# Performance work log

Hardware: AMD Instinct MI355X
Metric: run time of the kernel (lower is better)

## Reference

```python
import jax, jax.numpy as jnp
import numpy as np
from jax import lax

EMB, HID, L, PATCH, IMG, K = 192, 64, 6, 4, 224, 8
FMAP = IMG // PATCH
N = FMAP * FMAP
B = 8
ALG = 4
GB_np = np.array([0, 1, 1, 2])  # grade of each blade [1, e1, e2, e12]
GB = jnp.asarray(GB_np)

def _cayley_np():
    C = np.zeros((4, 4, 4), np.float32)
    tbl = {(0,0):(0,1.),(0,1):(1,1.),(0,2):(2,1.),(0,3):(3,1.),
           (1,0):(1,1.),(1,1):(0,1.),(1,2):(3,1.),(1,3):(2,1.),
           (2,0):(2,1.),(2,1):(3,-1.),(2,2):(0,1.),(2,3):(1,-1.),
           (3,0):(3,1.),(3,1):(2,-1.),(3,2):(1,1.),(3,3):(0,-1.)}
    for (i, j), (k, s) in tbl.items():
        C[i, j, k] = s
    return C

CAY_np = _cayley_np()
CAYLEY = jnp.asarray(CAY_np)
_paths = np.zeros((3, 3, 3), bool)
for _i in range(4):
    for _j in range(4):
        for _k in range(4):
            if CAY_np[_i, _j, _k] != 0:
                _paths[GB_np[_i], GB_np[_j], GB_np[_k]] = True
PI, PJ, PK = (jnp.asarray(a) for a in np.nonzero(_paths))
NPATH = int(_paths.sum())  # 10 geometric-product paths for Cl(2,0)

def build_knn_graph(H, W, k):
    yy, xx = np.meshgrid(np.arange(H, dtype=np.float32), np.arange(W, dtype=np.float32), indexing='ij')
    coords = np.stack([xx.ravel(), yy.ravel()], -1)
    cn = coords / np.array([W - 1, H - 1], np.float32) * 2 - 1
    d = np.linalg.norm(cn[:, None] - cn[None], axis=-1)
    np.fill_diagonal(d, np.inf)
    idx = np.argsort(d, axis=-1, kind='stable')[:, :k]
    rows = np.repeat(np.arange(H * W), k)
    cols = idx.reshape(-1)
    return rows.astype(np.int32), cols.astype(np.int32), cn.astype(np.float32)

def mvlin(x, W, b=None):
    # per-grade MVLinear: W [out,in,3] expanded to blades via GB
    y = jnp.einsum('nmi,bmi->bni', W[:, :, GB], x)
    if b is not None:
        y = y.at[:, :, 0].add(b)  # bias embedded in scalar blade only
    return y

def mvlin_flat(x, W, b):
    # subspaces=False MVLinear: same weight across blades
    y = jnp.einsum('nm,bmi->bni', W, x)
    return y.at[:, :, 0].add(b)

def mv_silu(x, a, b):
    # invariants: [scalar, q(grade1), q(grade2)]; gate = sigmoid(a*inv+b)
    inv = jnp.concatenate([x[..., :1], x[..., 1:2]**2 + x[..., 2:3]**2, x[..., 3:4]**2], -1)
    return jax.nn.sigmoid(a * inv + b)[..., GB] * x

def normalize_mv(x, a):
    q = jnp.concatenate([x[..., :1]**2, x[..., 1:2]**2 + x[..., 2:3]**2, x[..., 3:4]**2], -1)
    n = jnp.sqrt(q + 1e-12)
    d = jax.nn.sigmoid(a) * (n - 1.0) + 1.0
    return x / (d + 1e-6)[..., GB]

def sgp(x, Wl, bl, Wr, na, gw):
    # SteerableGeometricProductLayer
    xr = normalize_mv(mvlin(x, Wr), na)
    full = jnp.zeros((gw.shape[0], 3, 3, 3), x.dtype).at[:, PI, PJ, PK].set(gw)
    fb = full[:, GB][:, :, GB][:, :, :, GB]  # [feat,4,4,4]
    gp = jnp.einsum('bni,nijk,bnk->bnj', x, CAYLEY[None] * fb, xr)
    return (mvlin(x, Wl, bl) + gp) * np.float32(1.0 / np.sqrt(2.0))

def _forward(x, conv_w, conv_b, stem_g, stem_b, pos_embed, in_W, in_b, in_Wl, in_bl, in_Wr, in_na, in_gw, eg_eW, eg_eb, eg_sa, eg_sb, eg_nW, eg_nb, eg_Wl, eg_bl, eg_Wr, eg_na, eg_gw, eg_aa, eg_ab, out_W, out_b, on_g, on_b, cls_W, cls_b, coords, rows, cols):
    Bx = x.shape[0]
    # stem: strided conv + LayerNorm over (C,H,W)
    y = lax.conv_general_dilated(x, conv_w, (PATCH, PATCH), 'VALID', dimension_numbers=('NCHW', 'OIHW', 'NCHW')) + conv_b[None, :, None, None]
    mu = y.mean(axis=(1, 2, 3), keepdims=True)
    var = ((y - mu) ** 2).mean(axis=(1, 2, 3), keepdims=True)
    y = (y - mu) / jnp.sqrt(var + 1e-5) * stem_g[None] + stem_b[None]
    y = y + pos_embed
    feat = y.transpose(0, 2, 3, 1).reshape(Bx * N, EMB)
    # embed features in scalar blade, coordinates in vector blades e1,e2
    h = jnp.zeros((Bx * N, EMB + 1, ALG), x.dtype)
    h = h.at[:, :EMB, 0].set(feat)
    h = h.at[:, EMB, 1:3].set(jnp.tile(coords, (Bx, 1)))
    h = sgp(mvlin_flat(h, in_W, in_b), in_Wl, in_bl, in_Wr, in_na, in_gw)
    BN = Bx * N
    for i in range(L):
        m = mv_silu(mvlin(h[rows] - h[cols], eg_eW[i], eg_eb[i]), eg_sa[i], eg_sb[i])
        agg = jax.ops.segment_sum(m, rows, num_segments=BN)  # count computed but unused in original
        nu = mvlin(jnp.concatenate([h, agg], axis=1), eg_nW[i], eg_nb[i])
        out = mv_silu(sgp(nu, eg_Wl[i], eg_bl[i], eg_Wr[i], eg_na[i], eg_gw[i]), eg_aa[i], eg_ab[i])
        h = h + out if i > 0 else out
    s = mvlin_flat(h, out_W, out_b)[..., 0]
    mu2 = s.mean(-1, keepdims=True)
    v2 = ((s - mu2) ** 2).mean(-1, keepdims=True)
    s = (s - mu2) / jnp.sqrt(v2 + 1e-5) * on_g + on_b
    pooled = s.reshape(Bx, N, EMB).mean(axis=1)
    return pooled @ cls_W.T + cls_b

def setup_inputs() -> dict:
    key = jax.random.key(0)
    ks = iter(jax.random.split(key, 64))
    nrm = lambda shape, s=0.05: jax.random.normal(next(ks), shape, jnp.float32) * s
    rows, cols, cn = build_knn_graph(FMAP, FMAP, K)
    offs = np.arange(B, dtype=np.int32)[:, None] * N
    rows_b = (rows[None] + offs).reshape(-1)
    cols_b = (cols[None] + offs).reshape(-1)
    return dict(
        x=jax.random.normal(next(ks), (B, 3, IMG, IMG), jnp.float32),
        conv_w=nrm((EMB, 3, PATCH, PATCH)),
        conv_b=jnp.zeros((EMB,), jnp.float32),
        stem_g=jnp.ones((EMB, FMAP, FMAP), jnp.float32),
        stem_b=jnp.zeros((EMB, FMAP, FMAP), jnp.float32),
        pos_embed=nrm((1, EMB, FMAP, FMAP), 0.02),
        coords=jnp.asarray(cn),
        in_W=nrm((HID, EMB + 1)), in_b=jnp.zeros((HID,), jnp.float32),
        in_Wl=nrm((HID, HID, 3)), in_bl=jnp.zeros((HID,), jnp.float32),
        in_Wr=nrm((HID, HID, 3)), in_na=jnp.zeros((HID, 3), jnp.float32),
        in_gw=nrm((HID, NPATH), 0.2),
        eg_eW=nrm((L, HID, HID, 3)), eg_eb=jnp.zeros((L, HID), jnp.float32),
        eg_sa=jnp.ones((L, HID, 3), jnp.float32), eg_sb=jnp.zeros((L, HID, 3), jnp.float32),
        eg_nW=nrm((L, HID, 2 * HID, 3)), eg_nb=jnp.zeros((L, HID), jnp.float32),
        eg_Wl=nrm((L, HID, HID, 3)), eg_bl=jnp.zeros((L, HID), jnp.float32),
        eg_Wr=nrm((L, HID, HID, 3)), eg_na=jnp.zeros((L, HID, 3), jnp.float32),
        eg_gw=nrm((L, HID, NPATH), 0.2),
        eg_aa=jnp.ones((L, HID, 3), jnp.float32), eg_ab=jnp.zeros((L, HID, 3), jnp.float32),
        out_W=nrm((EMB, HID)), out_b=jnp.zeros((EMB,), jnp.float32),
        on_g=jnp.ones((EMB,), jnp.float32), on_b=jnp.zeros((EMB,), jnp.float32),
        cls_W=nrm((10, EMB), 0.02), cls_b=jnp.zeros((10,), jnp.float32),
        rows=jnp.asarray(rows_b), cols=jnp.asarray(cols_b),
    )

def reference(x, conv_w, conv_b, stem_g, stem_b, pos_embed, coords, in_W, in_b, in_Wl, in_bl, in_Wr, in_na, in_gw, eg_eW, eg_eb, eg_sa, eg_sb, eg_nW, eg_nb, eg_Wl, eg_bl, eg_Wr, eg_na, eg_gw, eg_aa, eg_ab, out_W, out_b, on_g, on_b, cls_W, cls_b, rows, cols):
    return _forward(x, conv_w, conv_b, stem_g, stem_b, pos_embed, in_W, in_b, in_Wl, in_bl, in_Wr, in_na, in_gw, eg_eW, eg_eb, eg_sa, eg_sb, eg_nW, eg_nb, eg_Wl, eg_bl, eg_Wr, eg_na, eg_gw, eg_aa, eg_ab, out_W, out_b, on_g, on_b, cls_W, cls_b, coords, rows, cols)
```

## Files before the change

kernel.cpp:

```cpp
#include <hip/hip_runtime.h>
#include <hip/hip_bf16.h>
#include <math.h>

#define EMBC   192
#define NLAY   6
#define IMGC   224
#define FMAPC  56
#define NNODE  3136
#define NBATCH 8
#define BNODES 25088
#define KNNE   8
#define NT     32
#define RSQRT2 0.70710678118654752f

__device__ __forceinline__ float sigm(float x){ return 1.0f/(1.0f+__expf(-x)); }

__global__ void k_repackw(const float* __restrict__ src, float* __restrict__ dst, int K){
  int l = blockIdx.y;
  size_t S = (size_t)64*K*3;
  int t = blockIdx.x*256 + threadIdx.x;
  if(t < (int)S){
    int j = t % 3; int r = t / 3;
    int ci = r % 8; int m = (r / 8) % K; int wid = r / (8*K);
    dst[l*S + (((size_t)wid*K + m)*8 + ci)*3 + j] =
      src[l*S + ((size_t)(wid*8+ci)*K + m)*3 + j];
  }
}
__global__ void k_repack1(const float* __restrict__ src, float* __restrict__ dst,
                          int R, int K){
  int t = blockIdx.x*256 + threadIdx.x;
  if(t < R*K){
    int m = t % K, r = t / K;
    dst[m*R + r] = src[r*K + m];
  }
}

__global__ void k_tr(const float* __restrict__ g, const float* __restrict__ sb,
                     const float* __restrict__ pe, float* __restrict__ g2,
                     float* __restrict__ pb2){
  int n = blockIdx.x; int c = threadIdx.x;
  g2[n*EMBC + c]  = g[c*NNODE + n];
  pb2[n*EMBC + c] = sb[c*NNODE + n] + pe[c*NNODE + n];
}

__global__ __launch_bounds__(256) void k_conv(const float* __restrict__ x,
    const float* __restrict__ cw, const float* __restrict__ cb,
    float* __restrict__ y0, float* __restrict__ parts){
  __shared__ float xs[2688];
  __shared__ float wsh[9216];
  __shared__ float red[512];
  int blk = blockIdx.x; int b = blk / FMAPC; int ph = blk % FMAPC;
  int tid = threadIdx.x;
  for(int t = tid; t < 9216; t += 256) wsh[t] = cw[t];
  for(int t = tid; t < 2688; t += 256){
    int r = t / IMGC; int w = t % IMGC;
    int ci = r >> 2, kh = r & 3;
    xs[t] = x[((size_t)(b*3 + ci)*IMGC + (ph*4 + kh))*IMGC + w];
  }
  __syncthreads();
  float s1 = 0.f, s2 = 0.f;
  for(int oi = tid; oi < FMAPC*EMBC; oi += 256){
    int pw = oi / EMBC; int c = oi % EMBC;
    float acc = cb[c];
    const float4* wv4 = (const float4*)(wsh + c*48);
    #pragma unroll
    for(int r = 0; r < 12; ++r){
      float4 xv = *((const float4*)(xs + r*IMGC + pw*4));
      float4 wv = wv4[r];
      acc += xv.x*wv.x + xv.y*wv.y + xv.z*wv.z + xv.w*wv.w;
    }
    y0[((size_t)(b*NNODE + ph*FMAPC + pw))*EMBC + c] = acc;
    s1 += acc; s2 += acc*acc;
  }
  red[tid] = s1; red[256+tid] = s2;
  __syncthreads();
  for(int st = 128; st > 0; st >>= 1){
    if(tid < st){ red[tid] += red[tid+st]; red[256+tid] += red[256+tid+st]; }
    __syncthreads();
  }
  if(tid == 0){ parts[blk*2] = red[0]; parts[blk*2+1] = red[256]; }
}

__global__ void k_stats(const float* __restrict__ parts, float* __restrict__ stats){
  int b = threadIdx.x;
  if(b < NBATCH){
    float S = 0.f, Q = 0.f;
    for(int j = 0; j < FMAPC; ++j){ S += parts[(b*FMAPC+j)*2]; Q += parts[(b*FMAPC+j)*2+1]; }
    float cnt = (float)(EMBC*NNODE);
    float mu = S/cnt;
    float var = Q/cnt - mu*mu;
    stats[b*2] = mu; stats[b*2+1] = rsqrtf(var + 1e-5f);
  }
}

__global__ __launch_bounds__(256,2) void k_embed(const float* __restrict__ y0,
    const float* __restrict__ stats, const float* __restrict__ g2,
    const float* __restrict__ pb2, const float* __restrict__ inWp,
    const float* __restrict__ inb, const float* __restrict__ coords,
    float* __restrict__ xmv){
  __shared__ float fs[64*193];
  int tid = threadIdx.x, lane = tid & 63;
  int wid = __builtin_amdgcn_readfirstlane(tid >> 6);
  int ch0 = wid << 4;
  int p0 = blockIdx.x * 64;
  int b = p0 / NNODE; int n0 = p0 - b*NNODE;
  float mu = stats[b*2], rstd = stats[b*2+1];
  for(int t = tid; t < 64*192; t += 256){
    int n = t / 192, c = t - n*192;
    int nn = n0 + n;
    fs[n*193 + c] = (y0[(size_t)(p0+n)*192 + c] - mu)*rstd*g2[nn*192+c] + pb2[nn*192+c];
  }
  __syncthreads();
  float acc[16];
  #pragma unroll
  for(int ci = 0; ci < 16; ++ci) acc[ci] = 0.f;
  #pragma unroll 2
  for(int m = 0; m < 192; ++m){
    float xm = fs[lane*193 + m];
    const float* wp = inWp + m*64 + ch0;
    #pragma unroll
    for(int ci = 0; ci < 16; ++ci) acc[ci] += wp[ci]*xm;
  }
  float cx = coords[(n0+lane)*2], cy = coords[(n0+lane)*2+1];
  #pragma unroll
  for(int ci = 0; ci < 16; ++ci){
    int ch = ch0 + ci;
    float wc = inWp[192*64 + ch];
    float4 v; v.x = acc[ci] + inb[ch]; v.y = wc*cx; v.z = wc*cy; v.w = 0.f;
    *((float4*)(xmv + ((size_t)(p0+lane)*64 + ch)*4)) = v;
  }
}

__device__ __forceinline__ void stage_x(float* xs, const float* __restrict__ g,
                                        int p0, int tid){
  #pragma unroll
  for(int t = tid; t < NT*64; t += 512){
    int n = t >> 6, m = t & 63;
    *((float4*)(xs + (n<<8) + (((m + n)&63)<<2))) =
      *((const float4*)(g + (((size_t)(p0+n))<<8) + (m<<2)));
  }
}
__device__ __forceinline__ void copyout(const float* xs, float* __restrict__ g,
                                        int p0, int tid){
  #pragma unroll
  for(int t = tid; t < NT*64; t += 512){
    int n = t >> 6, m = t & 63;
    float4 v = *((const float4*)(xs + (n<<8) + (((m + n)&63)<<2)));
    *((float4*)(g + (((size_t)(p0+n))<<8) + (m<<2))) = v;
  }
}
__device__ __forceinline__ void stage_w(float* wst, const float* __restrict__ Wp,
                                        int K, int moff, int tid){
  #pragma unroll
  for(int t = tid; t < 3072; t += 512){
    int c = t / 384, r = t - c*384;
    ((float4*)wst)[t] = ((const float4*)(Wp + ((size_t)(c*K + moff)*24)))[r];
  }
}
__device__ __forceinline__ void mm4(float (&acc)[4][4], const float* __restrict__ wst,
                                    const float* __restrict__ xrow, int wbase, int n){
  #pragma unroll 4
  for(int m = 0; m < 64; ++m){
    float4 xv = *((const float4*)(xrow + (((m + n)&63)<<2)));
    const float* wp = wst + wbase + m*24;
    float4 a = *((const float4*)(wp));
    float4 b = *((const float4*)(wp+4));
    float4 c = *((const float4*)(wp+8));
    acc[0][0] += a.x*xv.x; acc[0][1] += a.y*xv.y; acc[0][2] += a.y*xv.z; acc[0][3] += a.z*xv.w;
    acc[1][0] += a.w*xv.x; acc[1][1] += b.x*xv.y; acc[1][2] += b.x*xv.z; acc[1][3] += b.y*xv.w;
    acc[2][0] += b.z*xv.x; acc[2][1] += b.w*xv.y; acc[2][2] += b.w*xv.z; acc[2][3] += c.x*xv.w;
    acc[3][0] += c.y*xv.x; acc[3][1] += c.z*xv.y; acc[3][2] += c.z*xv.z; acc[3][3] += c.w*xv.w;
  }
}

__global__ __launch_bounds__(512,4) void k_sgp0(const float* __restrict__ src,
    float* __restrict__ h, float* __restrict__ zout,
    const float* __restrict__ Wlp, const float* __restrict__ bl,
    const float* __restrict__ Wrp, const float* __restrict__ na,
    const float* __restrict__ gw, const float* __restrict__ zWp){
  __shared__ float xs[NT*256];
  __shared__ float wst[12288];
  int tid = threadIdx.x, lane = tid & 63;
  int wid = __builtin_amdgcn_readfirstlane(tid >> 6);
  int n = lane & 31, s = lane >> 5;
  int s4 = s*4;
  int wbase = wid*1536 + s*12;
  int p0 = blockIdx.x * NT;
  const float* xrow = xs + (n<<8);
  stage_x(xs, src, p0, tid);
  stage_w(wst, Wlp, 64, 0, tid);
  __syncthreads();
  float accl[4][4], accr[4][4];
  #pragma unroll
  for(int ci = 0; ci < 4; ++ci)
    #pragma unroll
    for(int bi = 0; bi < 4; ++bi){ accl[ci][bi]=0.f; accr[ci][bi]=0.f; }
  mm4(accl, wst, xrow, wbase, n);
  __syncthreads();
  stage_w(wst, Wrp, 64, 0, tid);
  __syncthreads();
  mm4(accr, wst, xrow, wbase, n);
  float out[4][4];
  #pragma unroll
  for(int ci = 0; ci < 4; ++ci){
    int ch = (wid<<3) + s4 + ci;
    float yr0 = accr[ci][0], yr1 = accr[ci][1], yr2 = accr[ci][2], yr3 = accr[ci][3];
    float na0 = sigm(na[ch*3]), na1 = sigm(na[ch*3+1]), na2 = sigm(na[ch*3+2]);
    float d0 = na0*(sqrtf(yr0*yr0 + 1e-12f) - 1.f) + 1.f + 1e-6f;
    float d1 = na1*(sqrtf(yr1*yr1 + yr2*yr2 + 1e-12f) - 1.f) + 1.f + 1e-6f;
    float d2 = na2*(sqrtf(yr3*yr3 + 1e-12f) - 1.f) + 1.f + 1e-6f;
    float xr0 = yr0/d0, xr1 = yr1/d1, xr2 = yr2/d1, xr3 = yr3/d2;
    float4 xv = *((const float4*)(xrow + (((ch + n)&63)<<2)));
    const float* gwp = gw + ch*10;
    float gp0 = gwp[0]*xv.x*xr0 + gwp[3]*(xv.y*xr1 + xv.z*xr2) + gwp[7]*xv.w*xr3;
    float gp1 = gwp[1]*xv.x*xr1 + gwp[4]*xv.y*xr0 - gwp[5]*xv.z*xr3 - gwp[8]*xv.w*xr2;
    float gp2 = gwp[1]*xv.x*xr2 + gwp[4]*xv.z*xr0 + gwp[5]*xv.y*xr3 + gwp[8]*xv.w*xr1;
    float gp3 = gwp[2]*xv.x*xr3 + gwp[6]*(xv.y*xr2 - xv.z*xr1) - gwp[9]*xv.w*xr0;
    out[ci][0] = (accl[ci][0] + bl[ch] + gp0)*RSQRT2;
    out[ci][1] = (accl[ci][1] + gp1)*RSQRT2;
    out[ci][2] = (accl[ci][2] + gp2)*RSQRT2;
    out[ci][3] = (accl[ci][3] + gp3)*RSQRT2;
  }
  __syncthreads();
  #pragma unroll
  for(int ci = 0; ci < 4; ++ci){
    int ch = (wid<<3) + s4 + ci;
    float4 v; v.x=out[ci][0]; v.y=out[ci][1]; v.z=out[ci][2]; v.w=out[ci][3];
    *((float4*)(xs + (n<<8) + (((ch + n)&63)<<2))) = v;
  }
  __syncthreads();
  copyout(xs, h, p0, tid);
  stage_w(wst, zWp, 64, 0, tid);
  __syncthreads();
  float az[4][4];
  #pragma unroll
  for(int ci = 0; ci < 4; ++ci)
    #pragma unroll
    for(int bi = 0; bi < 4; ++bi) az[ci][bi] = 0.f;
  mm4(az, wst, xrow, wbase, n);
  __syncthreads();
  #pragma unroll
  for(int ci = 0; ci < 4; ++ci){
    int ch = (wid<<3) + s4 + ci;
    float4 v; v.x=az[ci][0]; v.y=az[ci][1]; v.z=az[ci][2]; v.w=az[ci][3];
    *((float4*)(xs + (n<<8) + (((ch + n)&63)<<2))) = v;
  }
  __syncthreads();
  copyout(xs, zout, p0, tid);
}

__global__ __launch_bounds__(512,4) void k_layer(
    float* __restrict__ h, const float* __restrict__ z,
    float* __restrict__ zout, const int* __restrict__ cols,
    const float* __restrict__ eb, const float* __restrict__ sa,
    const float* __restrict__ sb,
    const float* __restrict__ nWp, const float* __restrict__ nb,
    const float* __restrict__ Wlp, const float* __restrict__ bl,
    const float* __restrict__ Wrp, const float* __restrict__ na,
    const float* __restrict__ gw, const float* __restrict__ aa,
    const float* __restrict__ ab,
    const float* __restrict__ zWp, int mode){
  __shared__ float xs[NT*256];
  __shared__ float wst[12288];
  int tid = threadIdx.x, lane = tid & 63;
  int wid = __builtin_amdgcn_readfirstlane(tid >> 6);
  int n = lane & 31, s = lane >> 5;
  int s4 = s*4;
  int wbase = wid*1536 + s*12;
  int p0 = blockIdx.x * NT;
  const float* xrow = xs + (n<<8);
  float ag[4][4];
  {
    int ch = lane;
    float ebv = eb[ch];
    float a0 = sa[ch*3], a1 = sa[ch*3+1], a2 = sa[ch*3+2];
    float b0 = sb[ch*3], b1 = sb[ch*3+1], b2 = sb[ch*3+2];
    #pragma unroll
    for(int e = 0; e < 4; ++e){
      int p = p0 + wid*4 + e;
      float4 zo = *((const float4*)(z + ((size_t)p*64 + ch)*4));
      float ax=0.f, ay=0.f, az_=0.f, aw=0.f;
      #pragma unroll
      for(int k = 0; k < KNNE; ++k){
        int c = cols[p*KNNE + k];
        float4 zc = *((const float4*)(z + ((size_t)c*64 + ch)*4));
        float d0 = zo.x - zc.x + ebv;
        float d1 = zo.y - zc.y;
        float d2 = zo.z - zc.z;
        float d3 = zo.w - zc.w;
        float g0 = sigm(a0*d0 + b0);
        float g1 = sigm(a1*(d1*d1 + d2*d2) + b1);
        float g2v = sigm(a2*(d3*d3) + b2);
        ax += g0*d0; ay += g1*d1; az_ += g1*d2; aw += g2v*d3;
      }
      ag[e][0]=ax; ag[e][1]=ay; ag[e][2]=az_; ag[e][3]=aw;
    }
  }
  stage_x(xs, h, p0, tid);
  stage_w(wst, nWp, 128, 0, tid);
  __syncthreads();
  float acc[4][4];
  #pragma unroll
  for(int ci = 0; ci < 4; ++ci)
    #pragma unroll
    for(int bi = 0; bi < 4; ++bi) acc[ci][bi] = 0.f;
  mm4(acc, wst, xrow, wbase, n);
  float hres[4][4];
  if(mode == 2){
    #pragma unroll
    for(int ci = 0; ci < 4; ++ci){
      int ch = (wid<<3) + s4 + ci;
      float4 v = *((const float4*)(xrow + (((ch + n)&63)<<2)));
      hres[ci][0]=v.x; hres[ci][1]=v.y; hres[ci][2]=v.z; hres[ci][3]=v.w;
    }
  }
  __syncthreads();
  #pragma unroll
  for(int e = 0; e < 4; ++e){
    int nn = wid*4 + e;
    float4 v; v.x=ag[e][0]; v.y=ag[e][1]; v.z=ag[e][2]; v.w=ag[e][3];
    *((float4*)(xs + (nn<<8) + (((lane + nn)&63)<<2))) = v;
  }
  stage_w(wst, nWp, 128, 64, tid);
  __syncthreads();
  mm4(acc, wst, xrow, wbase, n);
  __syncthreads();
  #pragma unroll
  for(int ci = 0; ci < 4; ++ci){
    int ch = (wid<<3) + s4 + ci;
    acc[ci][0] += nb[ch];
    float4 v; v.x=acc[ci][0]; v.y=acc[ci][1]; v.z=acc[ci][2]; v.w=acc[ci][3];
    *((float4*)(xs + (n<<8) + (((ch + n)&63)<<2))) = v;
  }
  stage_w(wst, Wlp, 64, 0, tid);
  __syncthreads();
  float accl[4][4], accr[4][4];
  #pragma unroll
  for(int ci = 0; ci < 4; ++ci)
    #pragma unroll
    for(int bi = 0; bi < 4; ++bi){ accl[ci][bi]=0.f; accr[ci][bi]=0.f; }
  mm4(accl, wst, xrow, wbase, n);
  __syncthreads();
  stage_w(wst, Wrp, 64, 0, tid);
  __syncthreads();
  mm4(accr, wst, xrow, wbase, n);
  float out[4][4];
  #pragma unroll
  for(int ci = 0; ci < 4; ++ci){
    int ch = (wid<<3) + s4 + ci;
    float yr0 = accr[ci][0], yr1 = accr[ci][1], yr2 = accr[ci][2], yr3 = accr[ci][3];
    float na0 = sigm(na[ch*3]), na1 = sigm(na[ch*3+1]), na2 = sigm(na[ch*3+2]);
    float d0 = na0*(sqrtf(yr0*yr0 + 1e-12f) - 1.f) + 1.f + 1e-6f;
    float d1 = na1*(sqrtf(yr1*yr1 + yr2*yr2 + 1e-12f) - 1.f) + 1.f + 1e-6f;
    float d2 = na2*(sqrtf(yr3*yr3 + 1e-12f) - 1.f) + 1.f + 1e-6f;
    float xr0 = yr0/d0, xr1 = yr1/d1, xr2 = yr2/d1, xr3 = yr3/d2;
    float x0 = acc[ci][0], x1 = acc[ci][1], x2 = acc[ci][2], x3 = acc[ci][3];
    const float* gwp = gw + ch*10;
    float gp0 = gwp[0]*x0*xr0 + gwp[3]*(x1*xr1 + x2*xr2) + gwp[7]*x3*xr3;
    float gp1 = gwp[1]*x0*xr1 + gwp[4]*x1*xr0 - gwp[5]*x2*xr3 - gwp[8]*x3*xr2;
    float gp2 = gwp[1]*x0*xr2 + gwp[4]*x2*xr0 + gwp[5]*x1*xr3 + gwp[8]*x3*xr1;
    float gp3 = gwp[2]*x0*xr3 + gwp[6]*(x1*xr2 - x2*xr1) - gwp[9]*x3*xr0;
    float o0 = (accl[ci][0] + bl[ch] + gp0)*RSQRT2;
    float o1 = (accl[ci][1] + gp1)*RSQRT2;
    float o2 = (accl[ci][2] + gp2)*RSQRT2;
    float o3 = (accl[ci][3] + gp3)*RSQRT2;
    float g0 = sigm(aa[ch*3]*o0 + ab[ch*3]);
    float g1 = sigm(aa[ch*3+1]*(o1*o1 + o2*o2) + ab[ch*3+1]);
    float g2v = sigm(aa[ch*3+2]*(o3*o3) + ab[ch*3+2]);
    float v0 = g0*o0, v1 = g1*o1, v2 = g1*o2, v3 = g2v*o3;
    if(mode == 2){ v0 += hres[ci][0]; v1 += hres[ci][1]; v2 += hres[ci][2]; v3 += hres[ci][3]; }
    out[ci][0]=v0; out[ci][1]=v1; out[ci][2]=v2; out[ci][3]=v3;
  }
  __syncthreads();
  #pragma unroll
  for(int ci = 0; ci < 4; ++ci){
    int ch = (wid<<3) + s4 + ci;
    float4 v; v.x=out[ci][0]; v.y=out[ci][1]; v.z=out[ci][2]; v.w=out[ci][3];
    *((float4*)(xs + (n<<8) + (((ch + n)&63)<<2))) = v;
  }
  __syncthreads();
  copyout(xs, h, p0, tid);
  if(zWp != nullptr){
    stage_w(wst, zWp, 64, 0, tid);
    __syncthreads();
    float az[4][4];
    #pragma unroll
    for(int ci = 0; ci < 4; ++ci)
      #pragma unroll
      for(int bi = 0; bi < 4; ++bi) az[ci][bi] = 0.f;
    mm4(az, wst, xrow, wbase, n);
    __syncthreads();
    #pragma unroll
    for(int ci = 0; ci < 4; ++ci){
      int ch = (wid<<3) + s4 + ci;
      float4 v; v.x=az[ci][0]; v.y=az[ci][1]; v.z=az[ci][2]; v.w=az[ci][3];
      *((float4*)(xs + (n<<8) + (((ch + n)&63)<<2))) = v;
    }
    __syncthreads();
    copyout(xs, zout, p0, tid);
  }
}

__global__ __launch_bounds__(256,2) void k_head(const float* __restrict__ h,
    const float* __restrict__ oWp, const float* __restrict__ ob,
    const float* __restrict__ ong, const float* __restrict__ onb,
    float* __restrict__ s){
  __shared__ float hs[64*65];
  __shared__ float rr[512];
  int tid = threadIdx.x, lane = tid & 63;
  int wid = __builtin_amdgcn_readfirstlane(tid >> 6);
  int c0 = wid*48;
  int p0 = blockIdx.x * 64;
  for(int t = tid; t < 64*64; t += 256){
    int nn = t >> 6, c = t & 63;
    hs[nn*65 + c] = h[(((size_t)(p0+nn))*64 + c)*4];
  }
  __syncthreads();
  float a[48];
  #pragma unroll
  for(int ci = 0; ci < 48; ++ci) a[ci] = 0.f;
  #pragma unroll 2
  for(int m = 0; m < 64; ++m){
    float xm = hs[lane*65 + m];
    const float* wp = oWp + m*192 + c0;
    #pragma unroll
    for(int ci = 0; ci < 48; ++ci) a[ci] += wp[ci]*xm;
  }
  float s1 = 0.f, s2 = 0.f;
  #pragma unroll
  for(int ci = 0; ci < 48; ++ci){
    a[ci] += ob[c0+ci];
    s1 += a[ci]; s2 += a[ci]*a[ci];
  }
  rr[wid*64 + lane] = s1; rr[256 + wid*64 + lane] = s2;
  __syncthreads();
  float S = rr[lane] + rr[64+lane] + rr[128+lane] + rr[192+lane];
  float Q = rr[256+lane] + rr[320+lane] + rr[384+lane] + rr[448+lane];
  float mu = S*(1.0f/EMBC);
  float var = Q*(1.0f/EMBC) - mu*mu;
  float rstd = rsqrtf(var + 1e-5f);
  #pragma unroll
  for(int q = 0; q < 12; ++q){
    int c = c0 + q*4;
    float4 v;
    v.x = (a[q*4  ] - mu)*rstd*ong[c  ] + onb[c  ];
    v.y = (a[q*4+1] - mu)*rstd*ong[c+1] + onb[c+1];
    v.z = (a[q*4+2] - mu)*rstd*ong[c+2] + onb[c+2];
    v.w = (a[q*4+3] - mu)*rstd*ong[c+3] + onb[c+3];
    *((float4*)(s + (size_t)(p0+lane)*192 + c)) = v;
  }
}

__global__ void k_pool1(const float* __restrict__ s, float* __restrict__ pp){
  int blk = blockIdx.x;
  int b = blk >> 5, chunk = blk & 31;
  int c = threadIdx.x;
  float acc = 0.f;
  int n0 = chunk*98;
  for(int j = 0; j < 98; ++j) acc += s[((size_t)(b*NNODE + n0 + j))*EMBC + c];
  pp[(size_t)blk*EMBC + c] = acc;
}
__global__ void k_pool2(const float* __restrict__ pp, float* __restrict__ pooled){
  int b = blockIdx.x; int c = threadIdx.x;
  float acc = 0.f;
  for(int j = 0; j < 32; ++j) acc += pp[((size_t)(b*32 + j))*EMBC + c];
  pooled[b*EMBC + c] = acc * (1.0f/NNODE);
}

__global__ void k_cls(const float* __restrict__ pooled, const float* __restrict__ cW,
                      const float* __restrict__ cb, float* __restrict__ out){
  int tid = threadIdx.x;
  if(tid < NBATCH*10){
    int b = tid/10, k = tid%10;
    float acc = cb[k];
    for(int c = 0; c < EMBC; ++c) acc += pooled[b*EMBC + c]*cW[k*EMBC + c];
    out[tid] = acc;
  }
}

extern "C" void kernel_launch(void* const* d_in, const int* in_sizes, int n_in,
                              void* d_out, int out_size, void* d_ws, size_t ws_size,
                              hipStream_t stream){
  const float* x      = (const float*)d_in[0];
  const float* conv_w = (const float*)d_in[1];
  const float* conv_b = (const float*)d_in[2];
  const float* stem_g = (const float*)d_in[3];
  const float* stem_b = (const float*)d_in[4];
  const float* pos_e  = (const float*)d_in[5];
  const float* coords = (const float*)d_in[6];
  const float* inW    = (const float*)d_in[7];
  const float* inb    = (const float*)d_in[8];
  const float* inWl   = (const float*)d_in[9];
  const float* inbl   = (const float*)d_in[10];
  const float* inWr   = (const float*)d_in[11];
  const float* inna   = (const float*)d_in[12];
  const float* ingw   = (const float*)d_in[13];
  const float* eg_eW  = (const float*)d_in[14];
  const float* eg_eb  = (const float*)d_in[15];
  const float* eg_sa  = (const float*)d_in[16];
  const float* eg_sb  = (const float*)d_in[17];
  const float* eg_nW  = (const float*)d_in[18];
  const float* eg_nb  = (const float*)d_in[19];
  const float* eg_Wl  = (const float*)d_in[20];
  const float* eg_bl  = (const float*)d_in[21];
  const float* eg_Wr  = (const float*)d_in[22];
  const float* eg_na  = (const float*)d_in[23];
  const float* eg_gw  = (const float*)d_in[24];
  const float* eg_aa  = (const float*)d_in[25];
  const float* eg_ab  = (const float*)d_in[26];
  const float* outW   = (const float*)d_in[27];
  const float* outb   = (const float*)d_in[28];
  const float* ong    = (const float*)d_in[29];
  const float* onb    = (const float*)d_in[30];
  const float* clsW   = (const float*)d_in[31];
  const float* clsb   = (const float*)d_in[32];
  const int*   cols   = (const int*)d_in[34];

  float* ws = (float*)d_ws;
  size_t off = 0;
  float* hbuf  = ws + off; off += (size_t)BNODES*256;
  float* bigA  = ws + off; off += (size_t)BNODES*256;
  float* bigB  = ws + off; off += (size_t)BNODES*256;
  float* g2    = ws + off; off += (size_t)NNODE*EMBC;
  float* pb2   = ws + off; off += (size_t)NNODE*EMBC;
  float* parts = ws + off; off += 896;
  float* stats = ws + off; off += 16;
  float* pp    = ws + off; off += 256*EMBC;
  float* pooled= ws + off; off += NBATCH*EMBC;
  float* wpInW = ws + off; off += 193*64;
  float* wpOW  = ws + off; off += 64*192;
  float* wpInWl= ws + off; off += 12288;
  float* wpInWr= ws + off; off += 12288;
  float* wpEW  = ws + off; off += (size_t)NLAY*12288;
  float* wpWl  = ws + off; off += (size_t)NLAY*12288;
  float* wpWr  = ws + off; off += (size_t)NLAY*12288;
  float* wpNW  = ws + off; off += (size_t)NLAY*24576;
  float* y0    = bigB;

  const int NTILE = BNODES/NT;

  { dim3 g1((12352+255)/256); k_repack1<<<g1, 256, 0, stream>>>(inW,  wpInW, 64, 193); }
  { dim3 g1((12288+255)/256); k_repack1<<<g1, 256, 0, stream>>>(outW, wpOW, 192, 64); }
  { dim3 g3((12288+255)/256, 1); k_repackw<<<g3, 256, 0, stream>>>(inWl, wpInWl, 64); }
  { dim3 g3((12288+255)/256, 1); k_repackw<<<g3, 256, 0, stream>>>(inWr, wpInWr, 64); }
  { dim3 g3((12288+255)/256, NLAY); k_repackw<<<g3, 256, 0, stream>>>(eg_eW, wpEW, 64); }
  { dim3 g3((12288+255)/256, NLAY); k_repackw<<<g3, 256, 0, stream>>>(eg_Wl, wpWl, 64); }
  { dim3 g3((12288+255)/256, NLAY); k_repackw<<<g3, 256, 0, stream>>>(eg_Wr, wpWr, 64); }
  { dim3 g3((24576+255)/256, NLAY); k_repackw<<<g3, 256, 0, stream>>>(eg_nW, wpNW, 128); }

  k_tr   <<<NNODE, 192, 0, stream>>>(stem_g, stem_b, pos_e, g2, pb2);
  k_conv <<<NBATCH*FMAPC, 256, 0, stream>>>(x, conv_w, conv_b, y0, parts);
  k_stats<<<1, 64, 0, stream>>>(parts, stats);
  k_embed<<<BNODES/64, 256, 0, stream>>>(y0, stats, g2, pb2, wpInW, inb, coords, bigA);
  k_sgp0 <<<NTILE, 512, 0, stream>>>(bigA, hbuf, bigB, wpInWl, inbl, wpInWr,
                                     inna, ingw, wpEW);
  float* zcur = bigB;
  float* spare = bigA;
  for(int l = 0; l < NLAY; ++l){
    const float* zWn = (l < NLAY-1) ? (wpEW + (size_t)(l+1)*12288) : (const float*)nullptr;
    k_layer<<<NTILE, 512, 0, stream>>>(hbuf, zcur, spare, cols,
        eg_eb + l*64, eg_sa + l*192, eg_sb + l*192,
        wpNW + (size_t)l*24576, eg_nb + l*64,
        wpWl + (size_t)l*12288, eg_bl + l*64,
        wpWr + (size_t)l*12288, eg_na + l*192,
        eg_gw + l*640, eg_aa + l*192, eg_ab + l*192,
        zWn, (l==0)?1:2);
    if(l < NLAY-1){ float* t = zcur; zcur = spare; spare = t; }
  }
  k_head <<<BNODES/64, 256, 0, stream>>>(hbuf, wpOW, outb, ong, onb, spare);
  k_pool1<<<256, 192, 0, stream>>>(spare, pp);
  k_pool2<<<8, 192, 0, stream>>>(pp, pooled);
  k_cls  <<<1, 128, 0, stream>>>(pooled, clsW, clsb, (float*)d_out);
}
```

Before: 1.558 ms.

## Double node tile per block so each thread computes two node rows per weight load

Raises the node tile from 32 to 64 per block and has each thread accumulate two nodes (n and n+32) against the same weight fragment loaded from shared memory. This halves weight staging and shared-memory weight reads per node and halves the block count. Launch bounds drop to one block per CU-slot occupancy target, so register use roughly doubles, which may cut occupancy and latency hiding. The edge aggregation now processes 8 nodes per wave.

```diff
diff --git a/kernel.cpp b/kernel.cpp
--- a/kernel.cpp
+++ b/kernel.cpp
@@ -10,7 +10,7 @@
 #define NBATCH 8
 #define BNODES 25088
 #define KNNE   8
-#define NT     32
+#define NT     64
 #define RSQRT2 0.70710678118654752f
 
 __device__ __forceinline__ float sigm(float x){ return 1.0f/(1.0f+__expf(-x)); }
@@ -157,23 +157,30 @@
     ((float4*)wst)[t] = ((const float4*)(Wp + ((size_t)(c*K + moff)*24)))[r];
   }
 }
-__device__ __forceinline__ void mm4(float (&acc)[4][4], const float* __restrict__ wst,
-                                    const float* __restrict__ xrow, int wbase, int n){
+__device__ __forceinline__ void mm2(float (&p)[4][4], float (&q)[4][4],
+    const float* __restrict__ wst, const float* __restrict__ xr0,
+    const float* __restrict__ xr1, int wb, int n){
   #pragma unroll 4
   for(int m = 0; m < 64; ++m){
-    float4 xv = *((const float4*)(xrow + (((m + n)&63)<<2)));
-    const float* wp = wst + wbase + m*24;
-    float4 a = *((const float4*)(wp));
+    float4 x0 = *((const float4*)(xr0 + (((m + n)&63)<<2)));
+    float4 x1 = *((const float4*)(xr1 + (((m + n + 32)&63)<<2)));
+    const float* wp = wst + wb + m*24;
+    float4 a = *((const float4*)wp);
     float4 b = *((const float4*)(wp+4));
     float4 c = *((const float4*)(wp+8));
-    acc[0][0] += a.x*xv.x; acc[0][1] += a.y*xv.y; acc[0][2] += a.y*xv.z; acc[0][3] += a.z*xv.w;
-    acc[1][0] += a.w*xv.x; acc[1][1] += b.x*xv.y; acc[1][2] += b.x*xv.z; acc[1][3] += b.y*xv.w;
-    acc[2][0] += b.z*xv.x; acc[2][1] += b.w*xv.y; acc[2][2] += b.w*xv.z; acc[2][3] += c.x*xv.w;
-    acc[3][0] += c.y*xv.x; acc[3][1] += c.z*xv.y; acc[3][2] += c.z*xv.z; acc[3][3] += c.w*xv.w;
-  }
-}
-
-__global__ __launch_bounds__(512,4) void k_sgp0(const float* __restrict__ src,
+    p[0][0]+=a.x*x0.x; p[0][1]+=a.y*x0.y; p[0][2]+=a.y*x0.z; p[0][3]+=a.z*x0.w;
+    p[1][0]+=a.w*x0.x; p[1][1]+=b.x*x0.y; p[1][2]+=b.x*x0.z; p[1][3]+=b.y*x0.w;
+    p[2][0]+=b.z*x0.x; p[2][1]+=b.w*x0.y; p[2][2]+=b.w*x0.z; p[2][3]+=c.x*x0.w;
+    p[3][0]+=c.y*x0.x; p[3][1]+=c.z*x0.y; p[3][2]+=c.z*x0.z; p[3][3]+=c.w*x0.w;
+    q[0][0]+=a.x*x1.x; q[0][1]+=a.y*x1.y; q[0][2]+=a.y*x1.z; q[0][3]+=a.z*x1.w;
+    q[1][0]+=a.w*x1.x; q[1][1]+=b.x*x1.y; q[1][2]+=b.x*x1.z; q[1][3]+=b.y*x1.w;
+    q[2][0]+=b.z*x1.x; q[2][1]+=b.w*x1.y; q[2][2]+=b.w*x1.z; q[2][3]+=c.x*x1.w;
+    q[3][0]+=c.y*x1.x; q[3][1]+=c.z*x1.y; q[3][2]+=c.z*x1.z; q[3][3]+=c.w*x1.w;
+  }
+}
+#define ZERO44(A) { _Pragma("unroll") for(int _i=0;_i<4;++_i) _Pragma("unroll") for(int _j=0;_j<4;++_j) A[_i][_j]=0.f; }
+
+__global__ __launch_bounds__(512,1) void k_sgp0(const float* __restrict__ src,
     float* __restrict__ h, float* __restrict__ zout,
     const float* __restrict__ Wlp, const float* __restrict__ bl,
     const float* __restrict__ Wrp, const float* __restrict__ na,
@@ -183,73 +190,80 @@
   int tid = threadIdx.x, lane = tid & 63;
   int wid = __builtin_amdgcn_readfirstlane(tid >> 6);
   int n = lane & 31, s = lane >> 5;
-  int s4 = s*4;
-  int wbase = wid*1536 + s*12;
+  int ch0 = (wid<<3) + s*4;
+  int wb = wid*1536 + s*12;
   int p0 = blockIdx.x * NT;
-  const float* xrow = xs + (n<<8);
+  const float* xr0 = xs + (n<<8);
+  const float* xr1 = xs + ((n+32)<<8);
   stage_x(xs, src, p0, tid);
   stage_w(wst, Wlp, 64, 0, tid);
   __syncthreads();
-  float accl[4][4], accr[4][4];
-  #pragma unroll
-  for(int ci = 0; ci < 4; ++ci)
-    #pragma unroll
-    for(int bi = 0; bi < 4; ++bi){ accl[ci][bi]=0.f; accr[ci][bi]=0.f; }
-  mm4(accl, wst, xrow, wbase, n);
+  float lA[4][4], lB[4][4], rA[4][4], rB[4][4];
+  ZERO44(lA); ZERO44(lB); ZERO44(rA); ZERO44(rB);
+  mm2(lA, lB, wst, xr0, xr1, wb, n);
   __syncthreads();
   stage_w(wst, Wrp, 64, 0, tid);
   __syncthreads();
-  mm4(accr, wst, xrow, wbase, n);
-  float out[4][4];
+  mm2(rA, rB, wst, xr0, xr1, wb, n);
+  float oA[4][4], oB[4][4];
+  #pragma unroll
+  for(int j = 0; j < 2; ++j){
+    int nn = n + j*32;
+    #pragma unroll
+    for(int ci = 0; ci < 4; ++ci){
+      int ch = ch0 + ci;
+      float yr0 = j? rB[ci][0]:rA[ci][0], yr1 = j? rB[ci][1]:rA[ci][1];
+      float yr2 = j? rB[ci][2]:rA[ci][2], yr3 = j? rB[ci][3]:rA[ci][3];
+      float na0 = sigm(na[ch*3]), na1 = sigm(na[ch*3+1]), na2 = sigm(na[ch*3+2]);
+      float d0 = na0*(sqrtf(yr0*yr0 + 1e-12f) - 1.f) + 1.f + 1e-6f;
+      float d1 = na1*(sqrtf(yr1*yr1 + yr2*yr2 + 1e-12f) - 1.f) + 1.f + 1e-6f;
+      float d2 = na2*(sqrtf(yr3*yr3 + 1e-12f) - 1.f) + 1.f + 1e-6f;
+      float xq0 = yr0/d0, xq1 = yr1/d1, xq2 = yr2/d1, xq3 = yr3/d2;
+      float4 xv = *((const float4*)(xs + (nn<<8) + (((ch + nn)&63)<<2)));
+      const float* gwp = gw + ch*10;
+      float gp0 = gwp[0]*xv.x*xq0 + gwp[3]*(xv.y*xq1 + xv.z*xq2) + gwp[7]*xv.w*xq3;
+      float gp1 = gwp[1]*xv.x*xq1 + gwp[4]*xv.y*xq0 - gwp[5]*xv.z*xq3 - gwp[8]*xv.w*xq2;
+      float gp2 = gwp[1]*xv.x*xq2 + gwp[4]*xv.z*xq0 + gwp[5]*xv.y*xq3 + gwp[8]*xv.w*xq1;
+      float gp3 = gwp[2]*xv.x*xq3 + gwp[6]*(xv.y*xq2 - xv.z*xq1) - gwp[9]*xv.w*xq0;
+      float l0 = j? lB[ci][0]:lA[ci][0], l1 = j? lB[ci][1]:lA[ci][1];
+      float l2 = j? lB[ci][2]:lA[ci][2], l3 = j? lB[ci][3]:lA[ci][3];
+      float* o = j? oB[ci] : oA[ci];
+      o[0] = (l0 + bl[ch] + gp0)*RSQRT2;
+      o[1] = (l1 + gp1)*RSQRT2;
+      o[2] = (l2 + gp2)*RSQRT2;
+      o[3] = (l3 + gp3)*RSQRT2;
+    }
+  }
+  __syncthreads();
   #pragma unroll
   for(int ci = 0; ci < 4; ++ci){
-    int ch = (wid<<3) + s4 + ci;
-    float yr0 = accr[ci][0], yr1 = accr[ci][1], yr2 = accr[ci][2], yr3 = accr[ci][3];
-    float na0 = sigm(na[ch*3]), na1 = sigm(na[ch*3+1]), na2 = sigm(na[ch*3+2]);
-    float d0 = na0*(sqrtf(yr0*yr0 + 1e-12f) - 1.f) + 1.f + 1e-6f;
-    float d1 = na1*(sqrtf(yr1*yr1 + yr2*yr2 + 1e-12f) - 1.f) + 1.f + 1e-6f;
-    float d2 = na2*(sqrtf(yr3*yr3 + 1e-12f) - 1.f) + 1.f + 1e-6f;
-    float xr0 = yr0/d0, xr1 = yr1/d1, xr2 = yr2/d1, xr3 = yr3/d2;
-    float4 xv = *((const float4*)(xrow + (((ch + n)&63)<<2)));
-    const float* gwp = gw + ch*10;
-    float gp0 = gwp[0]*xv.x*xr0 + gwp[3]*(xv.y*xr1 + xv.z*xr2) + gwp[7]*xv.w*xr3;
-    float gp1 = gwp[1]*xv.x*xr1 + gwp[4]*xv.y*xr0 - gwp[5]*xv.z*xr3 - gwp[8]*xv.w*xr2;
-    float gp2 = gwp[1]*xv.x*xr2 + gwp[4]*xv.z*xr0 + gwp[5]*xv.y*xr3 + gwp[8]*xv.w*xr1;
-    float gp3 = gwp[2]*xv.x*xr3 + gwp[6]*(xv.y*xr2 - xv.z*xr1) - gwp[9]*xv.w*xr0;
-    out[ci][0] = (accl[ci][0] + bl[ch] + gp0)*RSQRT2;
-    out[ci][1] = (accl[ci][1] + gp1)*RSQRT2;
-    out[ci][2] = (accl[ci][2] + gp2)*RSQRT2;
-    out[ci][3] = (accl[ci][3] + gp3)*RSQRT2;
-  }
-  __syncthreads();
-  #pragma unroll
-  for(int ci = 0; ci < 4; ++ci){
-    int ch = (wid<<3) + s4 + ci;
-    float4 v; v.x=out[ci][0]; v.y=out[ci][1]; v.z=out[ci][2]; v.w=out[ci][3];
-    *((float4*)(xs + (n<<8) + (((ch + n)&63)<<2))) = v;
+    int ch = ch0 + ci;
+    float4 v0; v0.x=oA[ci][0]; v0.y=oA[ci][1]; v0.z=oA[ci][2]; v0.w=oA[ci][3];
+    *((float4*)(xs + (n<<8) + (((ch + n)&63)<<2))) = v0;
+    float4 v1; v1.x=oB[ci][0]; v1.y=oB[ci][1]; v1.z=oB[ci][2]; v1.w=oB[ci][3];
+    *((float4*)(xs + ((n+32)<<8) + (((ch + n + 32)&63)<<2))) = v1;
   }
   __syncthreads();
   copyout(xs, h, p0, tid);
   stage_w(wst, zWp, 64, 0, tid);
   __syncthreads();
-  float az[4][4];
-  #pragma unroll
-  for(int ci = 0; ci < 4; ++ci)
-    #pragma unroll
-    for(int bi = 0; bi < 4; ++bi) az[ci][bi] = 0.f;
-  mm4(az, wst, xrow, wbase, n);
+  float zA[4][4], zB[4][4];
+  ZERO44(zA); ZERO44(zB);
+  mm2(zA, zB, wst, xr0, xr1, wb, n);
   __syncthreads();
   #pragma unroll
   for(int ci = 0; ci < 4; ++ci){
-    int ch = (wid<<3) + s4 + ci;
-    float4 v; v.x=az[ci][0]; v.y=az[ci][1]; v.z=az[ci][2]; v.w=az[ci][3];
-    *((float4*)(xs + (n<<8) + (((ch + n)&63)<<2))) = v;
+    int ch = ch0 + ci;
+    float4 v0; v0.x=zA[ci][0]; v0.y=zA[ci][1]; v0.z=zA[ci][2]; v0.w=zA[ci][3];
+    *((float4*)(xs + (n<<8) + (((ch + n)&63)<<2))) = v0;
+    float4 v1; v1.x=zB[ci][0]; v1.y=zB[ci][1]; v1.z=zB[ci][2]; v1.w=zB[ci][3];
+    *((float4*)(xs + ((n+32)<<8) + (((ch + n + 32)&63)<<2))) = v1;
   }
   __syncthreads();
   copyout(xs, zout, p0, tid);
 }
 
-__global__ __launch_bounds__(512,4) void k_layer(
+__global__ __launch_bounds__(512,1) void k_layer(
     float* __restrict__ h, const float* __restrict__ z,
     float* __restrict__ zout, const int* __restrict__ cols,
     const float* __restrict__ eb, const float* __restrict__ sa,
@@ -265,19 +279,20 @@
   int tid = threadIdx.x, lane = tid & 63;
   int wid = __builtin_amdgcn_readfirstlane(tid >> 6);
   int n = lane & 31, s = lane >> 5;
-  int s4 = s*4;
-  int wbase = wid*1536 + s*12;
+  int ch0 = (wid<<3) + s*4;
+  int wb = wid*1536 + s*12;
   int p0 = blockIdx.x * NT;
-  const float* xrow = xs + (n<<8);
-  float ag[4][4];
+  const float* xr0 = xs + (n<<8);
+  const float* xr1 = xs + ((n+32)<<8);
+  float ag[8][4];
   {
     int ch = lane;
     float ebv = eb[ch];
     float a0 = sa[ch*3], a1 = sa[ch*3+1], a2 = sa[ch*3+2];
     float b0 = sb[ch*3], b1 = sb[ch*3+1], b2 = sb[ch*3+2];
     #pragma unroll
-    for(int e = 0; e < 4; ++e){
-      int p = p0 + wid*4 + e;
+    for(int e = 0; e < 8; ++e){
+      int p = p0 + wid*8 + e;
       float4 zo = *((const float4*)(z + ((size_t)p*64 + ch)*4));
       float ax=0.f, ay=0.f, az_=0.f, aw=0.f;
       #pragma unroll
@@ -299,102 +314,114 @@
   stage_x(xs, h, p0, tid);
   stage_w(wst, nWp, 128, 0, tid);
   __syncthreads();
-  float acc[4][4];
-  #pragma unroll
-  for(int ci = 0; ci < 4; ++ci)
-    #pragma unroll
-    for(int bi = 0; bi < 4; ++bi) acc[ci][bi] = 0.f;
-  mm4(acc, wst, xrow, wbase, n);
-  float hres[4][4];
+  float nuA[4][4], nuB[4][4];
+  ZERO44(nuA); ZERO44(nuB);
+  mm2(nuA, nuB, wst, xr0, xr1, wb, n);
+  float hrA[4][4], hrB[4][4];
   if(mode == 2){
     #pragma unroll
     for(int ci = 0; ci < 4; ++ci){
-      int ch = (wid<<3) + s4 + ci;
-      float4 v = *((const float4*)(xrow + (((ch + n)&63)<<2)));
-      hres[ci][0]=v.x; hres[ci][1]=v.y; hres[ci][2]=v.z; hres[ci][3]=v.w;
+      int ch = ch0 + ci;
+      float4 v0 = *((const float4*)(xr0 + (((ch + n)&63)<<2)));
+      float4 v1 = *((const float4*)(xr1 + (((ch + n + 32)&63)<<2)));
+      hrA[ci][0]=v0.x; hrA[ci][1]=v0.y; hrA[ci][2]=v0.z; hrA[ci][3]=v0.w;
+      hrB[ci][0]=v1.x; hrB[ci][1]=v1.y; hrB[ci][2]=v1.z; hrB[ci][3]=v1.w;
     }
   }
   __syncthreads();
   #pragma unroll
-  for(int e = 0; e < 4; ++e){
-    int nn = wid*4 + e;
+  for(int e = 0; e < 8; ++e){
+    int nn = wid*8 + e;
     float4 v; v.x=ag[e][0]; v.y=ag[e][1]; v.z=ag[e][2]; v.w=ag[e][3];
     *((float4*)(xs + (nn<<8) + (((lane + nn)&63)<<2))) = v;
   }
   stage_w(wst, nWp, 128, 64, tid);
   __syncthreads();
-  mm4(acc, wst, xrow, wbase, n);
+  mm2(nuA, nuB, wst, xr0, xr1, wb, n);
   __syncthreads();
   #pragma unroll
   for(int ci = 0; ci < 4; ++ci){
-    int ch = (wid<<3) + s4 + ci;
-    acc[ci][0] += nb[ch];
-    float4 v; v.x=acc[ci][0]; v.y=acc[ci][1]; v.z=acc[ci][2]; v.w=acc[ci][3];
-    *((float4*)(xs + (n<<8) + (((ch + n)&63)<<2))) = v;
+    int ch = ch0 + ci;
+    nuA[ci][0] += nb[ch]; nuB[ci][0] += nb[ch];
+    float4 v0; v0.x=nuA[ci][0]; v0.y=nuA[ci][1]; v0.z=nuA[ci][2]; v0.w=nuA[ci][3];
+    *((float4*)(xs + (n<<8) + (((ch + n)&63)<<2))) = v0;
+    float4 v1; v1.x=nuB[ci][0]; v1.y=nuB[ci][1]; v1.z=nuB[ci][2]; v1.w=nuB[ci][3];
+    *((float4*)(xs + ((n+32)<<8) + (((ch + n + 32)&63)<<2))) = v1;
   }
   stage_w(wst, Wlp, 64, 0, tid);
   __syncthreads();
-  float accl[4][4], accr[4][4];
-  #pragma unroll
-  for(int ci = 0; ci < 4; ++ci)
-    #pragma unroll
-    for(int bi = 0; bi < 4; ++bi){ accl[ci][bi]=0.f; accr[ci][bi]=0.f; }
-  mm4(accl, wst, xrow, wbase, n);
+  float lA[4][4], lB[4][4];
+  ZERO44(lA); ZERO44(lB);
+  mm2(lA, lB, wst, xr0, xr1, wb, n);
   __syncthreads();
   stage_w(wst, Wrp, 64, 0, tid);
   __syncthreads();
-  mm4(accr, wst, xrow, wbase, n);
-  float out[4][4];
+  float rA[4][4], rB[4][4];
+  ZERO44(rA); ZERO44(rB);
+  mm2(rA, rB, wst, xr0, xr1, wb, n);
+  float oA[4][4], oB[4][4];
+  #pragma unroll
+  for(int j = 0; j < 2; ++j){
+    #pragma unroll
+    for(int ci = 0; ci < 4; ++ci){
+      int ch = ch0 + ci;
+      float yr0 = j? rB[ci][0]:rA[ci][0], yr1 = j? rB[ci][1]:rA[ci][1];
+      float yr2 = j? rB[ci][2]:rA[ci][2], yr3 = j? rB[ci][3]:rA[ci][3];
+      float na0 = sigm(na[ch*3]), na1 = sigm(na[ch*3+1]), na2 = sigm(na[ch*3+2]);
+      float d0 = na0*(sqrtf(yr0*yr0 + 1e-12f) - 1.f) + 1.f + 1e-6f;
+      float d1 = na1*(sqrtf(yr1*yr1 + yr2*yr2 + 1e-12f) - 1.f) + 1.f + 1e-6f;
+      float d2 = na2*(sqrtf(yr3*yr3 + 1e-12f) - 1.f) + 1.f + 1e-6f;
+      float xq0 = yr0/d0, xq1 = yr1/d1, xq2 = yr2/d1, xq3 = yr3/d2;
+      float x0 = j? nuB[ci][0]:nuA[ci][0], x1 = j? nuB[ci][1]:nuA[ci][1];
+      float x2 = j? nuB[ci][2]:nuA[ci][2], x3 = j? nuB[ci][3]:nuA[ci][3];
+      const float* gwp = gw + ch*10;
+      float gp0 = gwp[0]*x0*xq0 + gwp[3]*(x1*xq1 + x2*xq2) + gwp[7]*x3*xq3;
+      float gp1 = gwp[1]*x0*xq1 + gwp[4]*x1*xq0 - gwp[5]*x2*xq3 - gwp[8]*x3*xq2;
+      float gp2 = gwp[1]*x0*xq2 + gwp[4]*x2*xq0 + gwp[5]*x1*xq3 + gwp[8]*x3*xq1;
+      float gp3 = gwp[2]*x0*xq3 + gwp[6]*(x1*xq2 - x2*xq1) - gwp[9]*x3*xq0;
+      float l0 = j? lB[ci][0]:lA[ci][0], l1 = j? lB[ci][1]:lA[ci][1];
+      float l2 = j? lB[ci][2]:lA[ci][2], l3 = j? lB[ci][3]:lA[ci][3];
+      float o0 = (l0 + bl[ch] + gp0)*RSQRT2;
+      float o1 = (l1 + gp1)*RSQRT2;
+      float o2 = (l2 + gp2)*RSQRT2;
+      float o3 = (l3 + gp3)*RSQRT2;
+      float g0 = sigm(aa[ch*3]*o0 + ab[ch*3]);
+      float g1 = sigm(aa[ch*3+1]*(o1*o1 + o2*o2) + ab[ch*3+1]);
+      float g2v = sigm(aa[ch*3+2]*(o3*o3) + ab[ch*3+2]);
+      float v0 = g0*o0, v1 = g1*o1, v2 = g1*o2, v3 = g2v*o3;
+      if(mode == 2){
+        if(j){ v0 += hrB[ci][0]; v1 += hrB[ci][1]; v2 += hrB[ci][2]; v3 += hrB[ci][3]; }
+        else { v0 += hrA[ci][0]; v1 += hrA[ci][1]; v2 += hrA[ci][2]; v3 += hrA[ci][3]; }
+      }
+      float* o = j? oB[ci] : oA[ci];
+      o[0]=v0; o[1]=v1; o[2]=v2; o[3]=v3;
+    }
+  }
+  __syncthreads();
   #pragma unroll
   for(int ci = 0; ci < 4; ++ci){
-    int ch = (wid<<3) + s4 + ci;
-    float yr0 = accr[ci][0], yr1 = accr[ci][1], yr2 = accr[ci][2], yr3 = accr[ci][3];
-    float na0 = sigm(na[ch*3]), na1 = sigm(na[ch*3+1]), na2 = sigm(na[ch*3+2]);
-    float d0 = na0*(sqrtf(yr0*yr0 + 1e-12f) - 1.f) + 1.f + 1e-6f;
-    float d1 = na1*(sqrtf(yr1*yr1 + yr2*yr2 + 1e-12f) - 1.f) + 1.f + 1e-6f;
-    float d2 = na2*(sqrtf(yr3*yr3 + 1e-12f) - 1.f) + 1.f + 1e-6f;
-    float xr0 = yr0/d0, xr1 = yr1/d1, xr2 = yr2/d1, xr3 = yr3/d2;
-    float x0 = acc[ci][0], x1 = acc[ci][1], x2 = acc[ci][2], x3 = acc[ci][3];
-    const float* gwp = gw + ch*10;
-    float gp0 = gwp[0]*x0*xr0 + gwp[3]*(x1*xr1 + x2*xr2) + gwp[7]*x3*xr3;
-    float gp1 = gwp[1]*x0*xr1 + gwp[4]*x1*xr0 - gwp[5]*x2*xr3 - gwp[8]*x3*xr2;
-    float gp2 = gwp[1]*x0*xr2 + gwp[4]*x2*xr0 + gwp[5]*x1*xr3 + gwp[8]*x3*xr1;
-    float gp3 = gwp[2]*x0*xr3 + gwp[6]*(x1*xr2 - x2*xr1) - gwp[9]*x3*xr0;
-    float o0 = (accl[ci][0] + bl[ch] + gp0)*RSQRT2;
-    float o1 = (accl[ci][1] + gp1)*RSQRT2;
-    float o2 = (accl[ci][2] + gp2)*RSQRT2;
-    float o3 = (accl[ci][3] + gp3)*RSQRT2;
-    float g0 = sigm(aa[ch*3]*o0 + ab[ch*3]);
-    float g1 = sigm(aa[ch*3+1]*(o1*o1 + o2*o2) + ab[ch*3+1]);
-    float g2v = sigm(aa[ch*3+2]*(o3*o3) + ab[ch*3+2]);
-    float v0 = g0*o0, v1 = g1*o1, v2 = g1*o2, v3 = g2v*o3;
-    if(mode == 2){ v0 += hres[ci][0]; v1 += hres[ci][1]; v2 += hres[ci][2]; v3 += hres[ci][3]; }
-    out[ci][0]=v0; out[ci][1]=v1; out[ci][2]=v2; out[ci][3]=v3;
-  }
-  __syncthreads();
-  #pragma unroll
-  for(int ci = 0; ci < 4; ++ci){
-    int ch = (wid<<3) + s4 + ci;
-    float4 v; v.x=out[ci][0]; v.y=out[ci][1]; v.z=out[ci][2]; v.w=out[ci][3];
-    *((float4*)(xs + (n<<8) + (((ch + n)&63)<<2))) = v;
+    int ch = ch0 + ci;
+    float4 v0; v0.x=oA[ci][0]; v0.y=oA[ci][1]; v0.z=oA[ci][2]; v0.w=oA[ci][3];
+    *((float4*)(xs + (n<<8) + (((ch + n)&63)<<2))) = v0;
+    float4 v1; v1.x=oB[ci][0]; v1.y=oB[ci][1]; v1.z=oB[ci][2]; v1.w=oB[ci][3];
+    *((float4*)(xs + ((n+32)<<8) + (((ch + n + 32)&63)<<2))) = v1;
   }
   __syncthreads();
   copyout(xs, h, p0, tid);
   if(zWp != nullptr){
     stage_w(wst, zWp, 64, 0, tid);
     __syncthreads();
-    float az[4][4];
-    #pragma unroll
-    for(int ci = 0; ci < 4; ++ci)
-      #pragma unroll
-      for(int bi = 0; bi < 4; ++bi) az[ci][bi] = 0.f;
-    mm4(az, wst, xrow, wbase, n);
+    float zA[4][4], zB[4][4];
+    ZERO44(zA); ZERO44(zB);
+    mm2(zA, zB, wst, xr0, xr1, wb, n);
     __syncthreads();
     #pragma unroll
     for(int ci = 0; ci < 4; ++ci){
-      int ch = (wid<<3) + s4 + ci;
-      float4 v; v.x=az[ci][0]; v.y=az[ci][1]; v.z=az[ci][2]; v.w=az[ci][3];
-      *((float4*)(xs + (n<<8) + (((ch + n)&63)<<2))) = v;
+      int ch = ch0 + ci;
+      float4 v0; v0.x=zA[ci][0]; v0.y=zA[ci][1]; v0.z=zA[ci][2]; v0.w=zA[ci][3];
+      *((float4*)(xs + (n<<8) + (((ch + n)&63)<<2))) = v0;
+      float4 v1; v1.x=zB[ci][0]; v1.y=zB[ci][1]; v1.z=zB[ci][2]; v1.w=zB[ci][3];
+      *((float4*)(xs + ((n+32)<<8) + (((ch + n + 32)&63)<<2))) = v1;
     }
     __syncthreads();
     copyout(xs, zout, p0, tid);
```

Result: slower. 1.637 ms (+5.1%).
